# Performance work log

Measured on AMD Instinct MI355X. Metric: run time of the kernel, lower is better.

## Reference

```python
import jax, jax.numpy as jnp
import numpy as np

N = 50000      # nodes in batched graph
E = 1600000    # edges (avg degree ~32)
D = 64         # feature width (features_dim = h_dim = out_dim)
R = 4          # num_rels (bond types)
L = 4          # RGCN layers: i2h + 2 hidden + h2o
B = 256        # graphs in the batch
NEG_SLOPE = 0.2


def setup_inputs() -> dict:
    key = jax.random.key(0)
    ks = jax.random.split(key, 12)
    h = jax.random.normal(ks[0], (N, D), jnp.float32)
    src = jax.random.randint(ks[1], (E,), 0, N, jnp.int32)
    dst = jax.random.randint(ks[2], (E,), 0, N, jnp.int32)
    etypes = jax.random.randint(ks[3], (E,), 0, R, jnp.int32)
    gids = jnp.sort(jax.random.randint(ks[4], (N,), 0, B, jnp.int32))
    Wrel = jax.random.normal(ks[5], (L, R, D, D), jnp.float32) * 0.05
    Wloop = jax.random.normal(ks[6], (L, D, D), jnp.float32) * 0.05
    brel = jnp.zeros((L, D), jnp.float32)
    Wg = jax.random.normal(ks[7], (D, D), jnp.float32) * 0.05
    al = jax.random.normal(ks[8], (D,), jnp.float32) * 0.05
    ar = jax.random.normal(ks[9], (D,), jnp.float32) * 0.05
    Wd = jax.random.normal(ks[10], (D, 1), jnp.float32) * 0.05
    bd = jnp.zeros((1,), jnp.float32)
    return dict(h=h, Wrel=Wrel, Wloop=Wloop, brel=brel, Wg=Wg, al=al, ar=ar,
                Wd=Wd, bd=bd, src=src, dst=dst, etypes=etypes, gids=gids)


def reference(h, Wrel, Wloop, brel, Wg, al, ar, Wd, bd, src, dst, etypes, gids):
    n = h.shape[0]
    # --- stacked RelGraphConv layers (basis regularizer with num_bases=num_rels
    # -> per-relation weight), self-loop + bias + ReLU, sum aggregation ---
    for l in range(Wrel.shape[0]):
        hr = jnp.einsum('nd,rdo->nro', h, Wrel[l])          # [N, R, D]
        msg = hr[src, etypes]                                # [E, D] gather
        agg = jax.ops.segment_sum(msg, dst, num_segments=n)  # [N, D] scatter-add
        h = jax.nn.relu(agg + h @ Wloop[l] + brel[l])
    # --- GATConv, 1 head ---
    z = h @ Wg                                               # [N, D]
    el = z @ al                                              # [N] a_l . z
    er = z @ ar                                              # [N] a_r . z
    e = jax.nn.leaky_relu(el[src] + er[dst], NEG_SLOPE)      # [E]
    m = jax.ops.segment_max(e, dst, num_segments=n)          # edge-softmax (stable)
    ex = jnp.exp(e - m[dst])
    den = jax.ops.segment_sum(ex, dst, num_segments=n)
    alpha = ex / jnp.maximum(den[dst], 1e-9)                 # [E]
    hg = jax.ops.segment_sum(alpha[:, None] * z[src], dst, num_segments=n)  # [N, D]
    # --- SumPooling over each graph, view [N,1,D] -> pooled [B,1,D] ---
    pooled = jax.ops.segment_sum(hg, gids, num_segments=B)[:, None, :]
    # --- dense head ---
    return pooled @ Wd + bd                                  # [B, 1, 1]
```

## Files before the change

kernel.cpp:

```cpp
#include <hip/hip_runtime.h>

#define DD 64
#define EPB 1024
#define NREP 8

typedef float f32x4 __attribute__((ext_vector_type(4)));
typedef __bf16 bf16x8 __attribute__((ext_vector_type(8)));

__device__ __forceinline__ unsigned enc_f32(float x) {
  unsigned u = __float_as_uint(x);
  return (u & 0x80000000u) ? ~u : (u | 0x80000000u);
}
__device__ __forceinline__ float dec_f32(unsigned k) {
  return (k & 0x80000000u) ? __uint_as_float(k ^ 0x80000000u)
                           : __uint_as_float(~k);
}
__device__ __forceinline__ unsigned f2bf(float x) {
  unsigned u = __float_as_uint(x);
  return (u + 0x7fffu + ((u >> 16) & 1u)) >> 16;
}
__device__ __forceinline__ void unpack8(const uint4 raw, float* v) {
  v[0] = __uint_as_float(raw.x << 16);
  v[1] = __uint_as_float(raw.x & 0xffff0000u);
  v[2] = __uint_as_float(raw.y << 16);
  v[3] = __uint_as_float(raw.y & 0xffff0000u);
  v[4] = __uint_as_float(raw.z << 16);
  v[5] = __uint_as_float(raw.z & 0xffff0000u);
  v[6] = __uint_as_float(raw.w << 16);
  v[7] = __uint_as_float(raw.w & 0xffff0000u);
}
__device__ __forceinline__ float4 unpack4(const uint2 r) {
  return make_float4(__uint_as_float(r.x << 16),
                     __uint_as_float(r.x & 0xffff0000u),
                     __uint_as_float(r.y << 16),
                     __uint_as_float(r.y & 0xffff0000u));
}
__device__ __forceinline__ bf16x8 as_bf16x8(uint4 u) {
  union {
    uint4 u;
    bf16x8 b;
  } cv;
  cv.u = u;
  return cv.b;
}

__global__ __launch_bounds__(256) void conv_bf16(const float* __restrict__ x,
                                                 ushort* __restrict__ xb,
                                                 int n4) {
  int i = blockIdx.x * 256 + threadIdx.x;
  if (i < n4) {
    float4 v = ((const float4*)x)[i];
    uint2 o;
    o.x = f2bf(v.x) | (f2bf(v.y) << 16);
    o.y = f2bf(v.z) | (f2bf(v.w) << 16);
    ((uint2*)xb)[i] = o;
  }
}

__global__ __launch_bounds__(256) void f2_coarse(
    const int* __restrict__ src, const int* __restrict__ dst,
    const int* __restrict__ et, int* __restrict__ gcur,
    unsigned* __restrict__ staging, int E) {
  __shared__ int lcnt[256];
  __shared__ int sc[256];
  __shared__ int lbase[256];
  __shared__ int gb[256];
  __shared__ unsigned rec[EPB];
  __shared__ unsigned char rbk[EPB];

  const int t = threadIdx.x;
  const int base = blockIdx.x * EPB;
  const int rep = blockIdx.x & (NREP - 1);
  const int bc = min(EPB, E - base);

  lcnt[t] = 0;
  __syncthreads();

  int d_[EPB / 256], se_[EPB / 256], rk_[EPB / 256];
#pragma unroll
  for (int k = 0; k < EPB / 256; ++k) {
    const int e = base + k * 256 + t;
    if (e < E) {
      const int d = dst[e];
      d_[k] = d;
      se_[k] = (src[e] << 2) | et[e];
      rk_[k] = atomicAdd(&lcnt[d >> 8], 1);
    } else {
      d_[k] = -1;
    }
  }
  __syncthreads();

  const int lv = lcnt[t];
  sc[t] = lv;
  __syncthreads();
#pragma unroll
  for (int off = 1; off < 256; off <<= 1) {
    const int add = (t >= off) ? sc[t - off] : 0;
    __syncthreads();
    sc[t] += add;
    __syncthreads();
  }
  lbase[t] = sc[t] - lv;
  gb[t] = lv ? atomicAdd(&gcur[rep * 256 + t], lv) : 0;
  __syncthreads();

#pragma unroll
  for (int k = 0; k < EPB / 256; ++k) {
    if (d_[k] >= 0) {
      const int cb = d_[k] >> 8;
      const int pos = lbase[cb] + rk_[k];
      rec[pos] = ((unsigned)(d_[k] & 255) << 24) | (unsigned)se_[k];
      rbk[pos] = (unsigned char)cb;
    }
  }
  __syncthreads();

  for (int idx = t; idx < bc; idx += 256) {
    const int cb = rbk[idx];
    staging[gb[cb] + (idx - lbase[cb])] = rec[idx];
  }
}

__global__ __launch_bounds__(256) void cscan2(const int* __restrict__ gcur,
                                              int* __restrict__ cbase,
                                              int* __restrict__ rowptr, int N,
                                              int E, int CAP, int CAP8) {
  __shared__ int s[256];
  const int t = threadIdx.x;
  int c = 0;
#pragma unroll
  for (int r = 0; r < NREP; ++r)
    c += gcur[r * 256 + t] - (t * CAP + r * CAP8);
  s[t] = c;
  __syncthreads();
#pragma unroll
  for (int off = 1; off < 256; off <<= 1) {
    const int add = (t >= off) ? s[t - off] : 0;
    __syncthreads();
    s[t] += add;
    __syncthreads();
  }
  cbase[t] = s[t] - c;
  if (t == 0) rowptr[N] = E;
}

__global__ __launch_bounds__(256) void f3_fine4(
    const unsigned* __restrict__ staging, const int* __restrict__ gcur,
    const int* __restrict__ cbase, int* __restrict__ rowptr,
    int* __restrict__ srcet, int N, int CAP, int CAP8) {
  __shared__ int hist[256];
  __shared__ int sc[256];
  __shared__ int lcur[256];
  __shared__ int before;
  const int cb = blockIdx.x >> 2;
  const int sub = blockIdx.x & 3;
  const int t = threadIdx.x;
  const int dlo = sub << 6;

  hist[t] = 0;
  if (t == 0) before = 0;
  __syncthreads();

  int myb = 0;
#pragma unroll 1
  for (int r = 0; r < NREP; ++r) {
    const int s0 = cb * CAP + r * CAP8;
    const int s1 = gcur[r * 256 + cb];
    for (int i = s0 + t; i < s1; i += 256) {
      const unsigned rc = staging[i];
      const int dl = (int)(rc >> 24);
      const int off = dl - dlo;
      if ((unsigned)off < 64u)
        atomicAdd(&hist[(off << 2) | (int)(rc & 3u)], 1);
      else if (dl < dlo)
        ++myb;
    }
  }
#pragma unroll
  for (int off = 32; off > 0; off >>= 1) myb += __shfl_down(myb, off);
  if ((t & 63) == 0 && myb) atomicAdd(&before, myb);
  __syncthreads();

  const int v = hist[t];
  sc[t] = v;
  __syncthreads();
#pragma unroll
  for (int off = 1; off < 256; off <<= 1) {
    const int add = (t >= off) ? sc[t - off] : 0;
    __syncthreads();
    sc[t] += add;
    __syncthreads();
  }
  const int base = cbase[cb] + before + sc[t] - v;
  lcur[t] = base;
  if ((t & 3) == 0) {
    const int dn = (cb << 8) + dlo + (t >> 2);
    if (dn < N) rowptr[dn] = base;
  }
  __syncthreads();

#pragma unroll 1
  for (int r = 0; r < NREP; ++r) {
    const int s0 = cb * CAP + r * CAP8;
    const int s1 = gcur[r * 256 + cb];
    for (int i = s0 + t; i < s1; i += 256) {
      const unsigned rc = staging[i];
      const int dl = (int)(rc >> 24);
      const int off = dl - dlo;
      if ((unsigned)off < 64u) {
        const int pos = atomicAdd(&lcur[(off << 2) | (int)(rc & 3u)], 1);
        srcet[pos] = (int)(rc & 0xFFFFFFu);
      }
    }
  }
}

#define ACCUM(se, v)                                                         \
  {                                                                          \
    const int r_ = (se) & 3;                                                 \
    if (r_ == 0) { a0.x += v.x; a0.y += v.y; a0.z += v.z; a0.w += v.w; }     \
    else if (r_ == 1) { a1.x += v.x; a1.y += v.y; a1.z += v.z; a1.w += v.w; }\
    else if (r_ == 2) { a2.x += v.x; a2.y += v.y; a2.z += v.z; a2.w += v.w; }\
    else { a3.x += v.x; a3.y += v.y; a3.z += v.z; a3.w += v.w; }             \
  }

__global__ __launch_bounds__(256) void gather_rel(
    const ushort* __restrict__ hb, const int* __restrict__ rowptr,
    const int* __restrict__ srcet, ushort* __restrict__ aggr_bf, int N) {
  const int n = blockIdx.x * 4 + (threadIdx.x >> 6);
  const int lane = threadIdx.x & 63;
  const int g = lane >> 4;
  const int t = lane & 15;
  if (n >= N) return;
  const int beg = rowptr[n], end = rowptr[n + 1];

  float4 a0 = make_float4(0.f, 0.f, 0.f, 0.f);
  float4 a1 = a0, a2 = a0, a3 = a0;

  int j = beg + g;
  for (; j + 12 < end; j += 16) {
    const int se0 = srcet[j];
    const int se1 = srcet[j + 4];
    const int se2 = srcet[j + 8];
    const int se3 = srcet[j + 12];
    const uint2 r0 = *(const uint2*)(hb + ((size_t)(se0 >> 2) << 6) + (t << 2));
    const uint2 r1 = *(const uint2*)(hb + ((size_t)(se1 >> 2) << 6) + (t << 2));
    const uint2 r2 = *(const uint2*)(hb + ((size_t)(se2 >> 2) << 6) + (t << 2));
    const uint2 r3 = *(const uint2*)(hb + ((size_t)(se3 >> 2) << 6) + (t << 2));
    const float4 v0 = unpack4(r0);
    const float4 v1 = unpack4(r1);
    const float4 v2 = unpack4(r2);
    const float4 v3 = unpack4(r3);
    ACCUM(se0, v0);
    ACCUM(se1, v1);
    ACCUM(se2, v2);
    ACCUM(se3, v3);
  }
  for (; j < end; j += 4) {
    const int se0 = srcet[j];
    const uint2 r0 = *(const uint2*)(hb + ((size_t)(se0 >> 2) << 6) + (t << 2));
    const float4 v0 = unpack4(r0);
    ACCUM(se0, v0);
  }

#pragma unroll
  for (int off = 16; off <= 32; off <<= 1) {
    a0.x += __shfl_xor(a0.x, off); a0.y += __shfl_xor(a0.y, off);
    a0.z += __shfl_xor(a0.z, off); a0.w += __shfl_xor(a0.w, off);
    a1.x += __shfl_xor(a1.x, off); a1.y += __shfl_xor(a1.y, off);
    a1.z += __shfl_xor(a1.z, off); a1.w += __shfl_xor(a1.w, off);
    a2.x += __shfl_xor(a2.x, off); a2.y += __shfl_xor(a2.y, off);
    a2.z += __shfl_xor(a2.z, off); a2.w += __shfl_xor(a2.w, off);
    a3.x += __shfl_xor(a3.x, off); a3.y += __shfl_xor(a3.y, off);
    a3.z += __shfl_xor(a3.z, off); a3.w += __shfl_xor(a3.w, off);
  }

  const float4 res = (g == 0) ? a0 : (g == 1) ? a1 : (g == 2) ? a2 : a3;
  uint2 p;
  p.x = f2bf(res.x) | (f2bf(res.y) << 16);
  p.y = f2bf(res.z) | (f2bf(res.w) << 16);
  *(uint2*)(aggr_bf + ((size_t)n << 8) + (g << 6) + (t << 2)) = p;
}

__global__ __launch_bounds__(256) void pack_w(
    const float* __restrict__ Wrel, const float* __restrict__ Wloop,
    const float* __restrict__ Wg, const float* __restrict__ al,
    const float* __restrict__ ar, const float* __restrict__ Wd,
    ushort* __restrict__ wpk, float* __restrict__ vav, int L) {
  const int l = blockIdx.x;
  if (l < L) {
    for (int f = threadIdx.x; f < 2560; f += 256) {
      const int lane = f & 63;
      const int kc = f >> 6;
      const int kt = kc >> 2;
      const int c = kc & 3;
      const int o = c * 16 + (lane & 15);
      const int kl0 = (lane >> 4) * 8;
      const float* wsrc =
          (kt < 8)
              ? Wrel + ((((size_t)l * 4 + (kt >> 1)) * 64 + (kt & 1) * 32 + kl0) * 64)
              : Wloop + (((size_t)l * 64 + (kt - 8) * 32 + kl0) * 64);
      unsigned o8[8];
#pragma unroll
      for (int j = 0; j < 8; ++j) o8[j] = f2bf(wsrc[(size_t)j * 64 + o]);
      uint4 p;
      p.x = o8[0] | (o8[1] << 16);
      p.y = o8[2] | (o8[3] << 16);
      p.z = o8[4] | (o8[5] << 16);
      p.w = o8[6] | (o8[7] << 16);
      *(uint4*)(wpk + (size_t)l * 20480 + (size_t)f * 8) = p;
    }
  } else {
    const int tt = threadIdx.x;
    if (tt < 192) {
      const int which = tt >> 6;
      const int d = tt & 63;
      const float* v = (which == 0) ? al : (which == 1) ? ar : Wd;
      float s = 0.f;
#pragma unroll
      for (int o = 0; o < 64; ++o) s = fmaf(Wg[d * 64 + o], v[o], s);
      vav[tt] = s;
    }
  }
}

__global__ __launch_bounds__(256) void rgcn_dense_mfma(
    const ushort* __restrict__ aggr_bf, const ushort* __restrict__ hb_in,
    const ushort* __restrict__ wpk, const float* __restrict__ bias,
    ushort* __restrict__ hb_out, int N) {
  __shared__ __align__(16) char smraw[40960];
  const int tid = threadIdx.x;

  {
    const uint4* gsrc = (const uint4*)wpk;
    uint4* ldst = (uint4*)smraw;
#pragma unroll
    for (int i = 0; i < 10; ++i) ldst[i * 256 + tid] = gsrc[i * 256 + tid];
  }

  const int w = tid >> 6;
  const int lane = tid & 63;
  const int t = lane & 15;
  const int g = lane >> 4;
  const int n = blockIdx.x * 64 + w * 16 + t;
  const bool valid = n < N;

  f32x4 acc[4];
#pragma unroll
  for (int c = 0; c < 4; ++c) {
    const float b = bias[c * 16 + t];
    f32x4 z = {b, b, b, b};
    acc[c] = z;
  }

  __syncthreads();
  const bf16x8* bfr = (const bf16x8*)smraw;

#pragma unroll
  for (int kt = 0; kt < 10; ++kt) {
    uint4 raw = make_uint4(0u, 0u, 0u, 0u);
    if (valid) {
      const ushort* ap =
          (kt < 8) ? aggr_bf + (((size_t)n) << 8) + (kt << 5) + (g << 3)
                   : hb_in + (((size_t)n) << 6) + ((kt - 8) << 5) + (g << 3);
      raw = *(const uint4*)ap;
    }
    const bf16x8 a = as_bf16x8(raw);
#pragma unroll
    for (int c = 0; c < 4; ++c) {
      acc[c] = __builtin_amdgcn_mfma_f32_16x16x32_bf16(
          a, bfr[(kt * 4 + c) * 64 + lane], acc[c], 0, 0, 0);
    }
  }

  __syncthreads();
  float* tile = (float*)smraw;
  {
    const int r0 = w * 16 + g * 4;
#pragma unroll
    for (int c = 0; c < 4; ++c) {
      const int col = c * 16 + t;
#pragma unroll
      for (int r = 0; r < 4; ++r)
        tile[(r0 + r) * 65 + col] = fmaxf(acc[c][r], 0.f);
    }
  }
  __syncthreads();
  const int n0 = blockIdx.x * 64;
#pragma unroll
  for (int q = 0; q < 2; ++q) {
    const int f = q * 256 + tid;
    const int row = f >> 3;
    const int c8 = (f & 7) << 3;
    const int nn = n0 + row;
    if (nn < N) {
      const float* s = tile + row * 65 + c8;
      uint4 p;
      p.x = f2bf(s[0]) | (f2bf(s[1]) << 16);
      p.y = f2bf(s[2]) | (f2bf(s[3]) << 16);
      p.z = f2bf(s[4]) | (f2bf(s[5]) << 16);
      p.w = f2bf(s[6]) | (f2bf(s[7]) << 16);
      *(uint4*)(hb_out + (((size_t)nn) << 6) + c8) = p;
    }
  }
}

__global__ __launch_bounds__(256) void gat_proj(
    const ushort* __restrict__ hb, const float* __restrict__ vav,
    float* __restrict__ el, float* __restrict__ er, float* __restrict__ yv,
    unsigned* __restrict__ genc, int N) {
  __shared__ float sv[192];
  const int tid = threadIdx.x;
  if (tid < 192) sv[tid] = vav[tid];
  __syncthreads();
  const int n = blockIdx.x * 256 + tid;
  float pl = 0.f, pr = 0.f, py = 0.f;
  if (n < N) {
    const ushort* row = hb + ((size_t)n << 6);
#pragma unroll
    for (int q = 0; q < 8; ++q) {
      const uint4 raw = *(const uint4*)(row + (q << 3));
      float v[8];
      unpack8(raw, v);
#pragma unroll
      for (int j = 0; j < 8; ++j) {
        pl = fmaf(v[j], sv[q * 8 + j], pl);
        pr = fmaf(v[j], sv[64 + q * 8 + j], pr);
        py = fmaf(v[j], sv[128 + q * 8 + j], py);
      }
    }
    el[n] = pl;
    er[n] = pr;
    yv[n] = py;
  }
  float mx = (n < N) ? pl : -1e30f;
#pragma unroll
  for (int off = 32; off > 0; off >>= 1) mx = fmaxf(mx, __shfl_xor(mx, off));
  if ((tid & 63) == 0) atomicMax(genc, enc_f32(mx));
}

#define GSC_NPG 2
#define GSC_NPB (16 * GSC_NPG)
__global__ __launch_bounds__(256) void gat_scalar(
    const float* __restrict__ el, const float* __restrict__ er,
    const float* __restrict__ y, const int* __restrict__ rowptr,
    const int* __restrict__ srcet, const unsigned* __restrict__ genc,
    const int* __restrict__ gids, float* __restrict__ out, int N, int B) {
  __shared__ float acc[256];
  for (int i = threadIdx.x; i < B; i += 256) acc[i] = 0.f;
  __syncthreads();
  const int grp = threadIdx.x >> 4;
  const int ln = threadIdx.x & 15;
  const float gmax = dec_f32(*genc);
  const int base = blockIdx.x * GSC_NPB + grp * GSC_NPG;

#pragma unroll
  for (int i = 0; i < GSC_NPG; ++i) {
    const int n = base + i;
    if (n < N) {
      const int beg = rowptr[n], end = rowptr[n + 1];
      const float ern = er[n];
      float mb = gmax + ern;
      mb = (mb > 0.f) ? mb : 0.2f * mb;
      float num = 0.f, den = 0.f;
      for (int j = beg + ln; j < end; j += 16) {
        const int s = srcet[j] >> 2;
        float x = el[s] + ern;
        x = (x > 0.f) ? x : 0.2f * x;
        const float w = __expf(x - mb);
        num = fmaf(w, y[s], num);
        den += w;
      }
#pragma unroll
      for (int off = 1; off < 16; off <<= 1) {
        num += __shfl_xor(num, off);
        den += __shfl_xor(den, off);
      }
      if (ln == 0) atomicAdd(&acc[gids[n]], num / fmaxf(den, 1e-9f));
    }
  }
  __syncthreads();
  for (int i = threadIdx.x; i < B; i += 256) {
    const float v = acc[i];
    if (v != 0.f) unsafeAtomicAdd(out + i, v);
  }
}

__global__ void init_out_k(float* out, const float* bd, int n, unsigned* genc,
                           int* gcur, int CAP, int CAP8) {
  int i = blockIdx.x * blockDim.x + threadIdx.x;
  if (i < n) out[i] = bd[0];
  if (i < 256 * NREP) {
    const int r = i >> 8;
    const int b = i & 255;
    gcur[i] = b * CAP + r * CAP8;
  }
  if (i == 0) *genc = enc_f32(-1e30f);
}

extern "C" void kernel_launch(void* const* d_in, const int* in_sizes, int n_in,
                              void* d_out, int out_size, void* d_ws,
                              size_t ws_size, hipStream_t stream) {
  const float* h0 = (const float*)d_in[0];
  const float* Wrel = (const float*)d_in[1];
  const float* Wloop = (const float*)d_in[2];
  const float* brel = (const float*)d_in[3];
  const float* Wg = (const float*)d_in[4];
  const float* al = (const float*)d_in[5];
  const float* ar = (const float*)d_in[6];
  const float* Wd = (const float*)d_in[7];
  const float* bd = (const float*)d_in[8];
  const int* src = (const int*)d_in[9];
  const int* dst = (const int*)d_in[10];
  const int* et = (const int*)d_in[11];
  const int* gids = (const int*)d_in[12];

  const int N = in_sizes[0] / DD;
  const int E = in_sizes[9];
  const int L = in_sizes[2] / (DD * DD);
  float* out = (float*)d_out;
  const int CAP8 = ((E / (256 * NREP)) * 2 + 63) & ~63;
  const int CAP = CAP8 * NREP;

  char* wsb = (char*)d_ws;
  ushort* hbA = (ushort*)wsb;
  ushort* hbB = hbA + (size_t)N * DD;
  ushort* aggr_bf = hbB + (size_t)N * DD;
  int* rowptr = (int*)(aggr_bf + (size_t)N * 256);
  int* srcet = rowptr + N + 1;
  float* el = (float*)(srcet + E);
  float* er = el + N;
  float* yv = er + N;
  int* gcur = (int*)(yv + N);
  int* cbase = gcur + 256 * NREP;
  unsigned* genc = (unsigned*)(cbase + 256);
  unsigned* staging = (unsigned*)aggr_bf;
  float* vav = (float*)(genc + 1);
  ushort* wpk = (ushort*)(((size_t)(char*)el + 15) & ~(size_t)15);

  dim3 b256(256);
  const int grid_dense = (N + 63) / 64;
  const int nfb = (E + EPB - 1) / EPB;
  const int ncb = (N + 255) >> 8;

  hipLaunchKernelGGL(init_out_k, dim3((max(out_size, 256 * NREP) + 255) / 256),
                     b256, 0, stream, out, bd, out_size, genc, gcur, CAP, CAP8);

  hipLaunchKernelGGL(pack_w, dim3(L + 1), b256, 0, stream, Wrel, Wloop, Wg, al,
                     ar, Wd, wpk, vav, L);

  hipLaunchKernelGGL(f2_coarse, dim3(nfb), b256, 0, stream, src, dst, et, gcur,
                     staging, E);
  hipLaunchKernelGGL(cscan2, dim3(1), b256, 0, stream, gcur, cbase, rowptr, N,
                     E, CAP, CAP8);
  hipLaunchKernelGGL(f3_fine4, dim3(ncb * 4), b256, 0, stream, staging, gcur,
                     cbase, rowptr, srcet, N, CAP, CAP8);

  hipLaunchKernelGGL(conv_bf16, dim3((N * DD / 4 + 255) / 256), b256, 0, stream,
                     h0, hbA, N * DD / 4);

  ushort* cur = hbA;
  ushort* nxt = hbB;
  for (int l = 0; l < L; ++l) {
    hipLaunchKernelGGL(gather_rel, dim3((N + 3) / 4), b256, 0, stream, cur,
                       rowptr, srcet, aggr_bf, N);
    hipLaunchKernelGGL(rgcn_dense_mfma, dim3(grid_dense), b256, 0, stream,
                       aggr_bf, cur, wpk + (size_t)l * 20480,
                       brel + (size_t)l * DD, nxt, N);
    ushort* tmp = cur; cur = nxt; nxt = tmp;
  }

  hipLaunchKernelGGL(gat_proj, dim3((N + 255) / 256), b256, 0, stream, cur, vav,
                     el, er, yv, genc, N);
  const int grid_gs = (N + GSC_NPB - 1) / GSC_NPB;
  hipLaunchKernelGGL(gat_scalar, dim3(grid_gs), b256, 0, stream, el, er, yv,
                     rowptr, srcet, genc, gids, out, N, out_size);
}
```

Before: 364.7 us.

## Fuse relational gather with MFMA dense layer and pack GAT el/y

Merges the per-layer gather kernel and the MFMA dense kernel into one 512-thread kernel. Each block gathers 64 nodes' per-relation aggregates into swizzled LDS and then runs the bf16 MFMA projection from LDS, so the 256-wide bf16 aggregate no longer round-trips through global memory. The gather loop is also unrolled to eight edges in flight. Separately, el and y are packed into one float2 so the GAT edge loop does a single gather per edge. The risk is that the 72KB of LDS per block and 512 threads may limit occupancy for the latency-bound gather phase.

```diff
diff --git a/kernel.cpp b/kernel.cpp
--- a/kernel.cpp
+++ b/kernel.cpp
@@ -214,73 +214,6 @@
       }
     }
   }
-}
-
-#define ACCUM(se, v)                                                         \
-  {                                                                          \
-    const int r_ = (se) & 3;                                                 \
-    if (r_ == 0) { a0.x += v.x; a0.y += v.y; a0.z += v.z; a0.w += v.w; }     \
-    else if (r_ == 1) { a1.x += v.x; a1.y += v.y; a1.z += v.z; a1.w += v.w; }\
-    else if (r_ == 2) { a2.x += v.x; a2.y += v.y; a2.z += v.z; a2.w += v.w; }\
-    else { a3.x += v.x; a3.y += v.y; a3.z += v.z; a3.w += v.w; }             \
-  }
-
-__global__ __launch_bounds__(256) void gather_rel(
-    const ushort* __restrict__ hb, const int* __restrict__ rowptr,
-    const int* __restrict__ srcet, ushort* __restrict__ aggr_bf, int N) {
-  const int n = blockIdx.x * 4 + (threadIdx.x >> 6);
-  const int lane = threadIdx.x & 63;
-  const int g = lane >> 4;
-  const int t = lane & 15;
-  if (n >= N) return;
-  const int beg = rowptr[n], end = rowptr[n + 1];
-
-  float4 a0 = make_float4(0.f, 0.f, 0.f, 0.f);
-  float4 a1 = a0, a2 = a0, a3 = a0;
-
-  int j = beg + g;
-  for (; j + 12 < end; j += 16) {
-    const int se0 = srcet[j];
-    const int se1 = srcet[j + 4];
-    const int se2 = srcet[j + 8];
-    const int se3 = srcet[j + 12];
-    const uint2 r0 = *(const uint2*)(hb + ((size_t)(se0 >> 2) << 6) + (t << 2));
-    const uint2 r1 = *(const uint2*)(hb + ((size_t)(se1 >> 2) << 6) + (t << 2));
-    const uint2 r2 = *(const uint2*)(hb + ((size_t)(se2 >> 2) << 6) + (t << 2));
-    const uint2 r3 = *(const uint2*)(hb + ((size_t)(se3 >> 2) << 6) + (t << 2));
-    const float4 v0 = unpack4(r0);
-    const float4 v1 = unpack4(r1);
-    const float4 v2 = unpack4(r2);
-    const float4 v3 = unpack4(r3);
-    ACCUM(se0, v0);
-    ACCUM(se1, v1);
-    ACCUM(se2, v2);
-    ACCUM(se3, v3);
-  }
-  for (; j < end; j += 4) {
-    const int se0 = srcet[j];
-    const uint2 r0 = *(const uint2*)(hb + ((size_t)(se0 >> 2) << 6) + (t << 2));
-    const float4 v0 = unpack4(r0);
-    ACCUM(se0, v0);
-  }
-
-#pragma unroll
-  for (int off = 16; off <= 32; off <<= 1) {
-    a0.x += __shfl_xor(a0.x, off); a0.y += __shfl_xor(a0.y, off);
-    a0.z += __shfl_xor(a0.z, off); a0.w += __shfl_xor(a0.w, off);
-    a1.x += __shfl_xor(a1.x, off); a1.y += __shfl_xor(a1.y, off);
-    a1.z += __shfl_xor(a1.z, off); a1.w += __shfl_xor(a1.w, off);
-    a2.x += __shfl_xor(a2.x, off); a2.y += __shfl_xor(a2.y, off);
-    a2.z += __shfl_xor(a2.z, off); a2.w += __shfl_xor(a2.w, off);
-    a3.x += __shfl_xor(a3.x, off); a3.y += __shfl_xor(a3.y, off);
-    a3.z += __shfl_xor(a3.z, off); a3.w += __shfl_xor(a3.w, off);
-  }
-
-  const float4 res = (g == 0) ? a0 : (g == 1) ? a1 : (g == 2) ? a2 : a3;
-  uint2 p;
-  p.x = f2bf(res.x) | (f2bf(res.y) << 16);
-  p.y = f2bf(res.z) | (f2bf(res.w) << 16);
-  *(uint2*)(aggr_bf + ((size_t)n << 8) + (g << 6) + (t << 2)) = p;
 }
 
 __global__ __launch_bounds__(256) void pack_w(
@@ -325,74 +258,175 @@
   }
 }
 
-__global__ __launch_bounds__(256) void rgcn_dense_mfma(
-    const ushort* __restrict__ aggr_bf, const ushort* __restrict__ hb_in,
-    const ushort* __restrict__ wpk, const float* __restrict__ bias,
-    ushort* __restrict__ hb_out, int N) {
-  __shared__ __align__(16) char smraw[40960];
+#define ACCUM(se, v)                                                         \
+  {                                                                          \
+    const int r_ = (se) & 3;                                                 \
+    if (r_ == 0) { a0.x += v.x; a0.y += v.y; a0.z += v.z; a0.w += v.w; }     \
+    else if (r_ == 1) { a1.x += v.x; a1.y += v.y; a1.z += v.z; a1.w += v.w; }\
+    else if (r_ == 2) { a2.x += v.x; a2.y += v.y; a2.z += v.z; a2.w += v.w; }\
+    else { a3.x += v.x; a3.y += v.y; a3.z += v.z; a3.w += v.w; }             \
+  }
+
+__global__ __launch_bounds__(512, 4) void rgcn_fused(
+    const ushort* __restrict__ hb_in, const int* __restrict__ rowptr,
+    const int* __restrict__ srcet, const ushort* __restrict__ wpk,
+    const float* __restrict__ bias, ushort* __restrict__ hb_out, int N) {
+  __shared__ __align__(16) char smW[40960];
+  __shared__ __align__(16) char smA[32768];
   const int tid = threadIdx.x;
-
-  {
-    const uint4* gsrc = (const uint4*)wpk;
-    uint4* ldst = (uint4*)smraw;
-#pragma unroll
-    for (int i = 0; i < 10; ++i) ldst[i * 256 + tid] = gsrc[i * 256 + tid];
-  }
-
   const int w = tid >> 6;
   const int lane = tid & 63;
+  const int g = lane >> 4;
   const int t = lane & 15;
-  const int g = lane >> 4;
-  const int n = blockIdx.x * 64 + w * 16 + t;
+  const int n0 = blockIdx.x * 64;
+
+  {
+    const uint4* gs = (const uint4*)wpk;
+    uint4* ld = (uint4*)smW;
+#pragma unroll
+    for (int i = 0; i < 5; ++i) ld[i * 512 + tid] = gs[i * 512 + tid];
+  }
+
+  for (int ni = 0; ni < 8; ++ni) {
+    const int nl = (w << 3) + ni;
+    const int n = n0 + nl;
+    float4 a0 = make_float4(0.f, 0.f, 0.f, 0.f);
+    float4 a1 = a0, a2 = a0, a3 = a0;
+    float4 res = a0;
+    if (n < N) {
+      const int beg = rowptr[n], end = rowptr[n + 1];
+      int j = beg + g;
+      for (; j + 28 < end; j += 32) {
+        const int se0 = srcet[j];
+        const int se1 = srcet[j + 4];
+        const int se2 = srcet[j + 8];
+        const int se3 = srcet[j + 12];
+        const int se4 = srcet[j + 16];
+        const int se5 = srcet[j + 20];
+        const int se6 = srcet[j + 24];
+        const int se7 = srcet[j + 28];
+        const uint2 r0 = *(const uint2*)(hb_in + ((size_t)(se0 >> 2) << 6) + (t << 2));
+        const uint2 r1 = *(const uint2*)(hb_in + ((size_t)(se1 >> 2) << 6) + (t << 2));
+        const uint2 r2 = *(const uint2*)(hb_in + ((size_t)(se2 >> 2) << 6) + (t << 2));
+        const uint2 r3 = *(const uint2*)(hb_in + ((size_t)(se3 >> 2) << 6) + (t << 2));
+        const uint2 r4 = *(const uint2*)(hb_in + ((size_t)(se4 >> 2) << 6) + (t << 2));
+        const uint2 r5 = *(const uint2*)(hb_in + ((size_t)(se5 >> 2) << 6) + (t << 2));
+        const uint2 r6 = *(const uint2*)(hb_in + ((size_t)(se6 >> 2) << 6) + (t << 2));
+        const uint2 r7 = *(const uint2*)(hb_in + ((size_t)(se7 >> 2) << 6) + (t << 2));
+        const float4 v0 = unpack4(r0);
+        const float4 v1 = unpack4(r1);
+        const float4 v2 = unpack4(r2);
+        const float4 v3 = unpack4(r3);
+        const float4 v4 = unpack4(r4);
+        const float4 v5 = unpack4(r5);
+        const float4 v6 = unpack4(r6);
+        const float4 v7 = unpack4(r7);
+        ACCUM(se0, v0);
+        ACCUM(se1, v1);
+        ACCUM(se2, v2);
+        ACCUM(se3, v3);
+        ACCUM(se4, v4);
+        ACCUM(se5, v5);
+        ACCUM(se6, v6);
+        ACCUM(se7, v7);
+      }
+      for (; j + 12 < end; j += 16) {
+        const int se0 = srcet[j];
+        const int se1 = srcet[j + 4];
+        const int se2 = srcet[j + 8];
+        const int se3 = srcet[j + 12];
+        const uint2 r0 = *(const uint2*)(hb_in + ((size_t)(se0 >> 2) << 6) + (t << 2));
+        const uint2 r1 = *(const uint2*)(hb_in + ((size_t)(se1 >> 2) << 6) + (t << 2));
+        const uint2 r2 = *(const uint2*)(hb_in + ((size_t)(se2 >> 2) << 6) + (t << 2));
+        const uint2 r3 = *(const uint2*)(hb_in + ((size_t)(se3 >> 2) << 6) + (t << 2));
+        const float4 v0 = unpack4(r0);
+        const float4 v1 = unpack4(r1);
+        const float4 v2 = unpack4(r2);
+        const float4 v3 = unpack4(r3);
+        ACCUM(se0, v0);
+        ACCUM(se1, v1);
+        ACCUM(se2, v2);
+        ACCUM(se3, v3);
+      }
+      for (; j < end; j += 4) {
+        const int se0 = srcet[j];
+        const uint2 r0 = *(const uint2*)(hb_in + ((size_t)(se0 >> 2) << 6) + (t << 2));
+        const float4 v0 = unpack4(r0);
+        ACCUM(se0, v0);
+      }
+#pragma unroll
+      for (int off = 16; off <= 32; off <<= 1) {
+        a0.x += __shfl_xor(a0.x, off); a0.y += __shfl_xor(a0.y, off);
+        a0.z += __shfl_xor(a0.z, off); a0.w += __shfl_xor(a0.w, off);
+        a1.x += __shfl_xor(a1.x, off); a1.y += __shfl_xor(a1.y, off);
+        a1.z += __shfl_xor(a1.z, off); a1.w += __shfl_xor(a1.w, off);
+        a2.x += __shfl_xor(a2.x, off); a2.y += __shfl_xor(a2.y, off);
+        a2.z += __shfl_xor(a2.z, off); a2.w += __shfl_xor(a2.w, off);
+        a3.x += __shfl_xor(a3.x, off); a3.y += __shfl_xor(a3.y, off);
+        a3.z += __shfl_xor(a3.z, off); a3.w += __shfl_xor(a3.w, off);
+      }
+      res = (g == 0) ? a0 : (g == 1) ? a1 : (g == 2) ? a2 : a3;
+    }
+    uint2 p;
+    p.x = f2bf(res.x) | (f2bf(res.y) << 16);
+    p.y = f2bf(res.z) | (f2bf(res.w) << 16);
+    const int sW = (g << 3) + (t >> 1);
+    const int sz = sW ^ (nl & 7);
+    *(uint2*)(smA + (nl << 9) + (sz << 4) + ((t & 1) << 3)) = p;
+  }
+  __syncthreads();
+
+  const int rt = w & 3;
+  const int c0_ = (w >> 2) << 1;
+  const int nr = (rt << 4) + t;
+  const int n = n0 + nr;
   const bool valid = n < N;
 
-  f32x4 acc[4];
-#pragma unroll
-  for (int c = 0; c < 4; ++c) {
-    const float b = bias[c * 16 + t];
+  f32x4 acc[2];
+#pragma unroll
+  for (int ci = 0; ci < 2; ++ci) {
+    const float b = bias[(c0_ + ci) * 16 + t];
     f32x4 z = {b, b, b, b};
-    acc[c] = z;
-  }
-
-  __syncthreads();
-  const bf16x8* bfr = (const bf16x8*)smraw;
-
+    acc[ci] = z;
+  }
+
+  const bf16x8* bw = (const bf16x8*)smW;
 #pragma unroll
   for (int kt = 0; kt < 10; ++kt) {
-    uint4 raw = make_uint4(0u, 0u, 0u, 0u);
-    if (valid) {
-      const ushort* ap =
-          (kt < 8) ? aggr_bf + (((size_t)n) << 8) + (kt << 5) + (g << 3)
-                   : hb_in + (((size_t)n) << 6) + ((kt - 8) << 5) + (g << 3);
-      raw = *(const uint4*)ap;
-    }
-    const bf16x8 a = as_bf16x8(raw);
-#pragma unroll
-    for (int c = 0; c < 4; ++c) {
-      acc[c] = __builtin_amdgcn_mfma_f32_16x16x32_bf16(
-          a, bfr[(kt * 4 + c) * 64 + lane], acc[c], 0, 0, 0);
-    }
-  }
-
-  __syncthreads();
-  float* tile = (float*)smraw;
+    bf16x8 a;
+    if (kt < 8) {
+      const int sl = ((kt << 2) + g) ^ (nr & 7);
+      a = *(const bf16x8*)(smA + (nr << 9) + (sl << 4));
+    } else {
+      uint4 raw = make_uint4(0u, 0u, 0u, 0u);
+      if (valid)
+        raw = *(const uint4*)(hb_in + (((size_t)n) << 6) + ((kt - 8) << 5) +
+                              (g << 3));
+      a = as_bf16x8(raw);
+    }
+#pragma unroll
+    for (int ci = 0; ci < 2; ++ci) {
+      acc[ci] = __builtin_amdgcn_mfma_f32_16x16x32_bf16(
+          a, bw[((kt << 2) + c0_ + ci) * 64 + lane], acc[ci], 0, 0, 0);
+    }
+  }
+
+  __syncthreads();
+  float* tile = (float*)smA;
   {
-    const int r0 = w * 16 + g * 4;
-#pragma unroll
-    for (int c = 0; c < 4; ++c) {
-      const int col = c * 16 + t;
+    const int r0 = (rt << 4) + (g << 2);
+#pragma unroll
+    for (int ci = 0; ci < 2; ++ci) {
+      const int col = (c0_ + ci) * 16 + t;
 #pragma unroll
       for (int r = 0; r < 4; ++r)
-        tile[(r0 + r) * 65 + col] = fmaxf(acc[c][r], 0.f);
-    }
-  }
-  __syncthreads();
-  const int n0 = blockIdx.x * 64;
-#pragma unroll
-  for (int q = 0; q < 2; ++q) {
-    const int f = q * 256 + tid;
-    const int row = f >> 3;
-    const int c8 = (f & 7) << 3;
+        tile[(r0 + r) * 65 + col] = fmaxf(acc[ci][r], 0.f);
+    }
+  }
+  __syncthreads();
+  {
+    const int row = tid >> 3;
+    const int c8 = (tid & 7) << 3;
     const int nn = n0 + row;
     if (nn < N) {
       const float* s = tile + row * 65 + c8;
@@ -408,7 +442,7 @@
 
 __global__ __launch_bounds__(256) void gat_proj(
     const ushort* __restrict__ hb, const float* __restrict__ vav,
-    float* __restrict__ el, float* __restrict__ er, float* __restrict__ yv,
+    float2* __restrict__ ely, float* __restrict__ er,
     unsigned* __restrict__ genc, int N) {
   __shared__ float sv[192];
   const int tid = threadIdx.x;
@@ -430,9 +464,8 @@
         py = fmaf(v[j], sv[128 + q * 8 + j], py);
       }
     }
-    el[n] = pl;
+    ely[n] = make_float2(pl, py);
     er[n] = pr;
-    yv[n] = py;
   }
   float mx = (n < N) ? pl : -1e30f;
 #pragma unroll
@@ -443,10 +476,10 @@
 #define GSC_NPG 2
 #define GSC_NPB (16 * GSC_NPG)
 __global__ __launch_bounds__(256) void gat_scalar(
-    const float* __restrict__ el, const float* __restrict__ er,
-    const float* __restrict__ y, const int* __restrict__ rowptr,
-    const int* __restrict__ srcet, const unsigned* __restrict__ genc,
-    const int* __restrict__ gids, float* __restrict__ out, int N, int B) {
+    const float2* __restrict__ ely, const float* __restrict__ er,
+    const int* __restrict__ rowptr, const int* __restrict__ srcet,
+    const unsigned* __restrict__ genc, const int* __restrict__ gids,
+    float* __restrict__ out, int N, int B) {
   __shared__ float acc[256];
   for (int i = threadIdx.x; i < B; i += 256) acc[i] = 0.f;
   __syncthreads();
@@ -465,11 +498,11 @@
       mb = (mb > 0.f) ? mb : 0.2f * mb;
       float num = 0.f, den = 0.f;
       for (int j = beg + ln; j < end; j += 16) {
-        const int s = srcet[j] >> 2;
-        float x = el[s] + ern;
+        const float2 e2 = ely[srcet[j] >> 2];
+        float x = e2.x + ern;
         x = (x > 0.f) ? x : 0.2f * x;
         const float w = __expf(x - mb);
-        num = fmaf(w, y[s], num);
+        num = fmaf(w, e2.y, num);
         den += w;
       }
 #pragma unroll
@@ -529,18 +562,17 @@
   ushort* aggr_bf = hbB + (size_t)N * DD;
   int* rowptr = (int*)(aggr_bf + (size_t)N * 256);
   int* srcet = rowptr + N + 1;
-  float* el = (float*)(srcet + E);
-  float* er = el + N;
-  float* yv = er + N;
-  int* gcur = (int*)(yv + N);
+  float2* ely = (float2*)(srcet + E);
+  float* er = (float*)(ely + N);
+  int* gcur = (int*)(er + N);
   int* cbase = gcur + 256 * NREP;
   unsigned* genc = (unsigned*)(cbase + 256);
   unsigned* staging = (unsigned*)aggr_bf;
   float* vav = (float*)(genc + 1);
-  ushort* wpk = (ushort*)(((size_t)(char*)el + 15) & ~(size_t)15);
+  ushort* wpk = (ushort*)(((size_t)(char*)ely + 15) & ~(size_t)15);
 
   dim3 b256(256);
-  const int grid_dense = (N + 63) / 64;
+  const int grid_tile = (N + 63) / 64;
   const int nfb = (E + EPB - 1) / EPB;
   const int ncb = (N + 255) >> 8;
 
@@ -563,17 +595,15 @@
   ushort* cur = hbA;
   ushort* nxt = hbB;
   for (int l = 0; l < L; ++l) {
-    hipLaunchKernelGGL(gather_rel, dim3((N + 3) / 4), b256, 0, stream, cur,
-                       rowptr, srcet, aggr_bf, N);
-    hipLaunchKernelGGL(rgcn_dense_mfma, dim3(grid_dense), b256, 0, stream,
-                       aggr_bf, cur, wpk + (size_t)l * 20480,
+    hipLaunchKernelGGL(rgcn_fused, dim3(grid_tile), dim3(512), 0, stream, cur,
+                       rowptr, srcet, wpk + (size_t)l * 20480,
                        brel + (size_t)l * DD, nxt, N);
     ushort* tmp = cur; cur = nxt; nxt = tmp;
   }
 
   hipLaunchKernelGGL(gat_proj, dim3((N + 255) / 256), b256, 0, stream, cur, vav,
-                     el, er, yv, genc, N);
+                     ely, er, genc, N);
   const int grid_gs = (N + GSC_NPB - 1) / GSC_NPB;
-  hipLaunchKernelGGL(gat_scalar, dim3(grid_gs), b256, 0, stream, el, er, yv,
+  hipLaunchKernelGGL(gat_scalar, dim3(grid_gs), b256, 0, stream, ely, er,
                      rowptr, srcet, genc, gids, out, N, out_size);
 }
```

Measured after the change: 634.6 us. +74.0%, slower.
